# Optimization experiments

Hardware: AMD Instinct MI355X
Metric: run time of the kernel (lower is better)

## Reference

```python
import jax, jax.numpy as jnp
import numpy as np

B, S, D, H = 4, 2048, 1024, 16
HD = D // H  # head dim = 64


def setup_inputs() -> dict:
    key = jax.random.key(0)
    ks = jax.random.split(key, 10)
    sd = 1.0 / np.sqrt(D)
    return {
        "x": jax.random.normal(ks[0], (B, S, D), jnp.float32),
        "Wq": jax.random.normal(ks[1], (D, D), jnp.float32) * sd,
        "Wk": jax.random.normal(ks[2], (D, D), jnp.float32) * sd,
        "Wv": jax.random.normal(ks[3], (D, D), jnp.float32) * sd,
        "in_w": jax.random.normal(ks[4], (3 * D, D), jnp.float32) * sd,
        "in_b": jax.random.normal(ks[5], (3 * D,), jnp.float32) * 0.01,
        "out_w": jax.random.normal(ks[6], (D, D), jnp.float32) * sd,
        "out_b": jax.random.normal(ks[7], (D,), jnp.float32) * 0.01,
        "proj_w": jax.random.normal(ks[8], (D, D), jnp.float32) * sd,
        "proj_b": jax.random.normal(ks[9], (D,), jnp.float32) * 0.01,
    }


def _attn_block(x, Wq, Wk, Wv, in_w, in_b, out_w, out_b, proj_w, proj_b):
    b, s, d = x.shape
    # redundant pre-projections (bias-free)
    q = jnp.einsum('bsd,ed->bse', x, Wq)
    k = jnp.einsum('bsd,ed->bse', x, Wk)
    v = jnp.einsum('bsd,ed->bse', x, Wv)
    # MultiheadAttention internal in-projection (with bias)
    wq, wk, wv = in_w[:d], in_w[d:2 * d], in_w[2 * d:]
    bq, bk, bv = in_b[:d], in_b[d:2 * d], in_b[2 * d:]
    Q = jnp.einsum('bse,fe->bsf', q, wq) + bq
    K = jnp.einsum('bse,fe->bsf', k, wk) + bk
    V = jnp.einsum('bse,fe->bsf', v, wv) + bv
    # split heads -> [b, h, s, hd]
    Q = Q.reshape(b, s, H, HD).transpose(0, 2, 1, 3)
    K = K.reshape(b, s, H, HD).transpose(0, 2, 1, 3)
    V = V.reshape(b, s, H, HD).transpose(0, 2, 1, 3)
    scale = 1.0 / np.sqrt(HD)
    scores = jnp.einsum('bhqd,bhkd->bhqk', Q * scale, K)
    # FAITHFUL quirk: float tril mask (ones / zeros) is ADDED to scores,
    # exactly as torch does with a float attn_mask (not a -inf causal mask).
    mask = jnp.tril(jnp.ones((s, s), scores.dtype))
    scores = scores + mask
    A = jax.nn.softmax(scores, axis=-1)
    ctx = jnp.einsum('bhqk,bhkd->bhqd', A, V)
    ctx = ctx.transpose(0, 2, 1, 3).reshape(b, s, d)
    attn = jnp.einsum('bse,fe->bsf', ctx, out_w) + out_b  # out_proj
    out = jnp.einsum('bse,fe->bsf', attn, proj_w) + proj_b  # self.project
    return x + out


def reference(x, Wq, Wk, Wv, in_w, in_b, out_w, out_b, proj_w, proj_b):
    return _attn_block(x, Wq, Wk, Wv, in_w, in_b, out_w, out_b, proj_w, proj_b)
```

## Files before the change

### kernel.cpp

```cpp
#include <hip/hip_runtime.h>
#include <stdint.h>

typedef unsigned short u16;
typedef __attribute__((ext_vector_type(8))) short bfx8;
typedef __attribute__((ext_vector_type(4))) float fx4;
typedef __attribute__((ext_vector_type(2))) unsigned int uint32x2;

static __device__ __forceinline__ u16 f2b(float f) {
  union { float f; uint32_t u; } v; v.f = f;
  uint32_t r = v.u + 0x7fffu + ((v.u >> 16) & 1u);
  return (u16)(r >> 16);
}

static __device__ __forceinline__ uint32_t cvtpk(float lo, float hi) {
  uint32_t r;
  asm("v_cvt_pk_bf16_f32 %0, %1, %2" : "=v"(r) : "v"(lo), "v"(hi));
  return r;
}

static __device__ __forceinline__ float ex2(float x) {
  float r;
  asm("v_exp_f32 %0, %1" : "=v"(r) : "v"(x));
  return r;
}

static __device__ __forceinline__ void gload16(const void* g, void* lds) {
  __builtin_amdgcn_global_load_lds((const __attribute__((address_space(1))) uint32_t*)g,
                                   (__attribute__((address_space(3))) uint32_t*)lds,
                                   16, 0, 0);
}

__global__ __launch_bounds__(256) void f32_to_bf16_k(const float* __restrict__ in,
                                                     u16* __restrict__ out, int n) {
  int i = (blockIdx.x * 256 + threadIdx.x) * 8;
  if (i >= n) return;
  float4 a = *(const float4*)(in + i);
  float4 b = *(const float4*)(in + i + 4);
  bfx8 o;
  o[0]=(short)f2b(a.x); o[1]=(short)f2b(a.y); o[2]=(short)f2b(a.z); o[3]=(short)f2b(a.w);
  o[4]=(short)f2b(b.x); o[5]=(short)f2b(b.y); o[6]=(short)f2b(b.z); o[7]=(short)f2b(b.w);
  *(bfx8*)(out + i) = o;
}

struct TransArgs { const float* in[4]; u16* out[4]; };
__global__ __launch_bounds__(256) void transpose4_k(TransArgs ta) {
  const float* in = ta.in[blockIdx.z];
  u16* out = ta.out[blockIdx.z];
  __shared__ u16 t[64][65];
  const int bx = blockIdx.x * 64, by = blockIdx.y * 64;
  const int tid = threadIdx.x;
#pragma unroll
  for (int i = 0; i < 16; ++i) {
    int idx = tid + i * 256; int r = idx >> 6, c = idx & 63;
    t[c][r] = f2b(in[(size_t)(by + r) * 1024 + bx + c]);
  }
  __syncthreads();
#pragma unroll
  for (int i = 0; i < 16; ++i) {
    int idx = tid + i * 256; int r = idx >> 6, c = idx & 63;
    out[(size_t)(bx + r) * 1024 + by + c] = t[r][c];
  }
}

__global__ __launch_bounds__(256) void make_b2_k(const float* __restrict__ pw,
                                                 const float* __restrict__ ob,
                                                 const float* __restrict__ pb,
                                                 float* __restrict__ b2) {
  const int f = blockIdx.x, tid = threadIdx.x;
  float s = 0.f;
  for (int e = tid; e < 1024; e += 256) s += pw[(size_t)f * 1024 + e] * ob[e];
#pragma unroll
  for (int d = 1; d < 64; d <<= 1) s += __shfl_xor(s, d);
  __shared__ float red[4];
  if ((tid & 63) == 0) red[tid >> 6] = s;
  __syncthreads();
  if (tid == 0) b2[f] = red[0] + red[1] + red[2] + red[3] + pb[f];
}

static __device__ __forceinline__ void gemm_core(const u16* __restrict__ A,
                                                 const u16* __restrict__ Bt,
                                                 int K, int bm, int bn,
                                                 u16* As, u16* Bs, fx4 (&acc)[4][4]) {
  const int tid = threadIdx.x, w = tid >> 6, l = tid & 63, lm = l & 15, lk = l >> 4;
  const int wm = w >> 1, wn = w & 1;
  const int nkt = K >> 6;
  for (int kt = 0; kt < nkt; ++kt) {
#pragma unroll
    for (int i = 0; i < 4; ++i) {
      int off = i * 4096 + w * 1024;
      int loff = off + l * 16;
      int row = loff >> 7, cb = loff & 127;
      gload16((const char*)A + ((size_t)(bm * 128 + row) * K + kt * 64) * 2 + cb,
              (char*)As + off);
      gload16((const char*)Bt + ((size_t)(bn * 128 + row) * K + kt * 64) * 2 + cb,
              (char*)Bs + off);
    }
    __syncthreads();
#pragma unroll
    for (int kk = 0; kk < 2; ++kk) {
      bfx8 a[4], b[4];
#pragma unroll
      for (int mi = 0; mi < 4; ++mi)
        a[mi] = *(const bfx8*)((const char*)As + (wm * 64 + mi * 16 + lm) * 128 + lk * 16 + kk * 64);
#pragma unroll
      for (int nj = 0; nj < 4; ++nj)
        b[nj] = *(const bfx8*)((const char*)Bs + (wn * 64 + nj * 16 + lm) * 128 + lk * 16 + kk * 64);
#pragma unroll
      for (int mi = 0; mi < 4; ++mi)
#pragma unroll
        for (int nj = 0; nj < 4; ++nj)
          acc[mi][nj] = __builtin_amdgcn_mfma_f32_16x16x32_bf16(a[mi], b[nj], acc[mi][nj], 0, 0, 0);
    }
    __syncthreads();
  }
}

struct CombArgs { const u16* A[4]; const u16* Bt[4]; u16* C[4]; };
__global__ __launch_bounds__(256) void gemm_combine_k(CombArgs ca) {
  const int z = blockIdx.z;
  __shared__ u16 As[8192], Bs[8192];
  fx4 acc[4][4];
#pragma unroll
  for (int mi = 0; mi < 4; ++mi)
#pragma unroll
    for (int nj = 0; nj < 4; ++nj) acc[mi][nj] = 0.f;
  gemm_core(ca.A[z], ca.Bt[z], 1024, blockIdx.x, blockIdx.y, As, Bs, acc);
  const int tid = threadIdx.x, w = tid >> 6, l = tid & 63, lm = l & 15, lk = l >> 4;
  const int wm = w >> 1, wn = w & 1;
  u16* C = ca.C[z];
#pragma unroll
  for (int mi = 0; mi < 4; ++mi)
#pragma unroll
    for (int nj = 0; nj < 4; ++nj)
#pragma unroll
      for (int r = 0; r < 4; ++r) {
        int m = blockIdx.x * 128 + wm * 64 + mi * 16 + lk * 4 + r;
        int n = blockIdx.y * 128 + wn * 64 + nj * 16 + lm;
        C[(size_t)m * 1024 + n] = f2b(acc[mi][nj][r]);
      }
}

__global__ __launch_bounds__(256) void gemm_qkv_k(const u16* __restrict__ xb,
                                                  const u16* __restrict__ Wc,
                                                  const float* __restrict__ bias,
                                                  u16* __restrict__ Qh, u16* __restrict__ Kh,
                                                  u16* __restrict__ Vh) {
  __shared__ u16 As[8192], Bs[8192];
  fx4 acc[4][4];
#pragma unroll
  for (int mi = 0; mi < 4; ++mi)
#pragma unroll
    for (int nj = 0; nj < 4; ++nj) acc[mi][nj] = 0.f;
  gemm_core(xb, Wc, 1024, blockIdx.x, blockIdx.y, As, Bs, acc);
  const int tid = threadIdx.x, w = tid >> 6, l = tid & 63, lm = l & 15, lk = l >> 4;
  const int wm = w >> 1, wn = w & 1;
  const int t = (blockIdx.y * 128) >> 10;
  u16* dst = (t == 0) ? Qh : ((t == 1) ? Kh : Vh);
#pragma unroll
  for (int mi = 0; mi < 4; ++mi)
#pragma unroll
    for (int nj = 0; nj < 4; ++nj)
#pragma unroll
      for (int r = 0; r < 4; ++r) {
        int m = blockIdx.x * 128 + wm * 64 + mi * 16 + lk * 4 + r;
        int n = blockIdx.y * 128 + wn * 64 + nj * 16 + lm;
        float v = acc[mi][nj][r] + bias[n];
        int f = n & 1023, h = f >> 6, hd = f & 63, b = m >> 11, s = m & 2047;
        size_t hb = ((size_t)(b * 16 + h)) * 131072;
        size_t idx;
        if (t == 2) {
          int sl = s & 63, st = s >> 6;
          idx = hb + (size_t)st * 4096 +
                (size_t)((sl >> 2) * 256 + (hd >> 4) * 64 + (sl & 3) * 16 + (hd & 15));
        } else if (t == 1) {
          idx = hb + (size_t)s * 64 + (hd ^ ((s & 7) << 3));
        } else {
          idx = hb + (size_t)s * 64 + hd;
        }
        dst[idx] = f2b(v);
      }
}

__global__ __launch_bounds__(256) void gemm_final_k(const u16* __restrict__ ctx,
                                                    const u16* __restrict__ W2,
                                                    const float* __restrict__ b2,
                                                    const float* __restrict__ x,
                                                    float* __restrict__ out) {
  __shared__ u16 As[8192], Bs[8192];
  fx4 acc[4][4];
#pragma unroll
  for (int mi = 0; mi < 4; ++mi)
#pragma unroll
    for (int nj = 0; nj < 4; ++nj) acc[mi][nj] = 0.f;
  gemm_core(ctx, W2, 1024, blockIdx.x, blockIdx.y, As, Bs, acc);
  const int tid = threadIdx.x, w = tid >> 6, l = tid & 63, lm = l & 15, lk = l >> 4;
  const int wm = w >> 1, wn = w & 1;
#pragma unroll
  for (int mi = 0; mi < 4; ++mi)
#pragma unroll
    for (int nj = 0; nj < 4; ++nj)
#pragma unroll
      for (int r = 0; r < 4; ++r) {
        int m = blockIdx.x * 128 + wm * 64 + mi * 16 + lk * 4 + r;
        int n = blockIdx.y * 128 + wn * 64 + nj * 16 + lm;
        size_t idx = (size_t)m * 1024 + n;
        out[idx] = acc[mi][nj][r] + b2[n] + x[idx];
      }
}

#define TRRD(d, IMM) asm volatile("ds_read_b64_tr_b16 %0, %1 offset:" IMM : "=v"(d) : "v"(va))

__global__ __launch_bounds__(256) void attn_k(const u16* __restrict__ Qh,
                                              const u16* __restrict__ Kh,
                                              const u16* __restrict__ Vh,
                                              u16* __restrict__ ctx) {
  const int bl = blockIdx.x;
  const int wk = (bl & 7) * 128 + (bl >> 3);
  const int bh = wk >> 4, qt = wk & 15;
  const int tid = threadIdx.x, w = tid >> 6, l = tid & 63, lm = l & 15, lk = l >> 4;
  __shared__ __align__(16) u16 Ks[3][4096];
  __shared__ __align__(16) u16 Vs[3][4096];
  __shared__ __align__(16) u16 Pl[4][1024];

  const float SC = 0.18033688011112042f;
  const float MA = 1.4426950408889634f;
  const float THR = 11.541560327111708f;

  const size_t base = (size_t)bh * 131072;
  bfx8 qf[2][2];
#pragma unroll
  for (int g = 0; g < 2; ++g) {
    const u16* qp = Qh + base + (size_t)(qt * 128 + g * 64 + w * 16 + lm) * 64;
    qf[g][0] = *(const bfx8*)(qp + lk * 8);
    qf[g][1] = *(const bfx8*)(qp + lk * 8 + 32);
  }
  float m_run[2] = {-INFINITY, -INFINITY};
  float l_part[2] = {0.f, 0.f};
  fx4 accO[2][4];
#pragma unroll
  for (int g = 0; g < 2; ++g)
#pragma unroll
    for (int nj = 0; nj < 4; ++nj) accO[g][nj] = 0.f;

  const char* Kg = (const char*)(Kh + base);
  const char* Vg = (const char*)(Vh + base);
  const int o0 = w * 1024 + l * 16, o1 = o0 + 4096;

  const int swz = (lm & 7) << 4;
  const uint32_t vs_base =
      (uint32_t)(uintptr_t)(__attribute__((address_space(3))) char*)&Vs[0][0];
  const uint32_t vtrb = vs_base + (uint32_t)(lk * 1024 + lm * 8);

#define STAGE(t, s)                                        \
  {                                                        \
    const char* kg_ = Kg + (t) * 8192;                     \
    const char* vg_ = Vg + (t) * 8192;                     \
    gload16(kg_ + o0, (char*)Ks[s] + o0);                  \
    gload16(kg_ + o1, (char*)Ks[s] + o1);                  \
    gload16(vg_ + o0, (char*)Vs[s] + o0);                  \
    gload16(vg_ + o1, (char*)Vs[s] + o1);                  \
  }

  STAGE(0, 0);
  STAGE(1, 1);
  asm volatile("s_waitcnt vmcnt(4)" ::: "memory");
  __builtin_amdgcn_s_barrier();
  __builtin_amdgcn_sched_barrier(0);

  int s0 = 0, s1 = 1, s2 = 2;
  for (int kt = 0; kt < 32; ++kt) {
    if (kt + 2 < 32) STAGE(kt + 2, s2);
    __builtin_amdgcn_sched_barrier(0);

    const char* Kc = (const char*)Ks[s0];
    fx4 s[2][4];
#pragma unroll
    for (int g = 0; g < 2; ++g)
#pragma unroll
      for (int nj = 0; nj < 4; ++nj) s[g][nj] = 0.f;
    __builtin_amdgcn_s_setprio(1);
#pragma unroll
    for (int kk = 0; kk < 2; ++kk) {
      bfx8 kf[4];
#pragma unroll
      for (int nj = 0; nj < 4; ++nj)
        kf[nj] = *(const bfx8*)(Kc + nj * 2048 + lm * 128 +
                                (((kk * 4 + lk) ^ (lm & 7)) << 4));
#pragma unroll
      for (int g = 0; g < 2; ++g)
#pragma unroll
        for (int nj = 0; nj < 4; ++nj)
          s[g][nj] = __builtin_amdgcn_mfma_f32_16x16x32_bf16(kf[nj], qf[g][kk], s[g][nj], 0, 0, 0);
    }
    __builtin_amdgcn_s_setprio(0);
#pragma unroll
    for (int g = 0; g < 2; ++g) {
      const int dk = kt - 2 * qt - g;
      if (dk < 0) {
#pragma unroll
        for (int nj = 0; nj < 4; ++nj)
#pragma unroll
          for (int r = 0; r < 4; ++r) s[g][nj][r] = fmaf(s[g][nj][r], SC, MA);
      } else if (dk > 0) {
#pragma unroll
        for (int nj = 0; nj < 4; ++nj)
#pragma unroll
          for (int r = 0; r < 4; ++r) s[g][nj][r] *= SC;
      } else {
        const int qg = qt * 128 + g * 64 + w * 16 + lm;
#pragma unroll
        for (int nj = 0; nj < 4; ++nj)
#pragma unroll
          for (int r = 0; r < 4; ++r) {
            int key = kt * 64 + nj * 16 + lk * 4 + r;
            s[g][nj][r] = s[g][nj][r] * SC + ((key <= qg) ? MA : 0.0f);
          }
      }
      float mx = fmaxf(fmaxf(fmaxf(s[g][0][0], s[g][0][1]), fmaxf(s[g][0][2], s[g][0][3])),
                       fmaxf(fmaxf(s[g][1][0], s[g][1][1]), fmaxf(s[g][1][2], s[g][1][3])));
      mx = fmaxf(mx, fmaxf(fmaxf(fmaxf(s[g][2][0], s[g][2][1]), fmaxf(s[g][2][2], s[g][2][3])),
                           fmaxf(fmaxf(s[g][3][0], s[g][3][1]), fmaxf(s[g][3][2], s[g][3][3]))));
      if (!__all(mx <= m_run[g] + THR)) {
        mx = fmaxf(mx, __shfl_xor(mx, 16));
        mx = fmaxf(mx, __shfl_xor(mx, 32));
        float mn = fmaxf(m_run[g], mx);
        float corr = ex2(m_run[g] - mn);
        m_run[g] = mn;
        l_part[g] *= corr;
#pragma unroll
        for (int r = 0; r < 4; ++r) {
          float cr = __shfl(corr, (l & 48) | (lk * 4 + r));
#pragma unroll
          for (int nj = 0; nj < 4; ++nj) accO[g][nj][r] *= cr;
        }
      }
      float lsum = 0.f;
#pragma unroll
      for (int nj = 0; nj < 4; ++nj)
#pragma unroll
        for (int r = 0; r < 4; ++r) {
          float p = ex2(s[g][nj][r] - m_run[g]);
          s[g][nj][r] = p;
          lsum += p;
        }
      l_part[g] += lsum;
    }
#pragma unroll
    for (int nj = 0; nj < 4; ++nj) {
      uint32x2 pw;
      pw[0] = cvtpk(s[0][nj][0], s[0][nj][1]);
      pw[1] = cvtpk(s[0][nj][2], s[0][nj][3]);
      *(uint32x2*)((char*)Pl[w] + ((lm * 128 + nj * 32 + lk * 8) ^ swz)) = pw;
    }
    uint32x2 tr[2][4][2];
    uint32_t va = vtrb + (uint32_t)(s0 * 8192);
    TRRD(tr[0][0][0], "0");    TRRD(tr[0][0][1], "512");
    TRRD(tr[0][1][0], "128");  TRRD(tr[0][1][1], "640");
    TRRD(tr[0][2][0], "256");  TRRD(tr[0][2][1], "768");
    TRRD(tr[0][3][0], "384");  TRRD(tr[0][3][1], "896");
    TRRD(tr[1][0][0], "4096"); TRRD(tr[1][0][1], "4608");
    TRRD(tr[1][1][0], "4224"); TRRD(tr[1][1][1], "4736");
    TRRD(tr[1][2][0], "4352"); TRRD(tr[1][2][1], "4864");
    TRRD(tr[1][3][0], "4480"); TRRD(tr[1][3][1], "4992");
    asm volatile("s_waitcnt lgkmcnt(0)" ::: "memory");
    __builtin_amdgcn_sched_barrier(0);
    __builtin_amdgcn_s_setprio(1);
#pragma unroll
    for (int kk = 0; kk < 2; ++kk) {
      bfx8 pf = *(const bfx8*)((char*)Pl[w] + ((lm * 128 + kk * 64 + lk * 16) ^ swz));
#pragma unroll
      for (int nj = 0; nj < 4; ++nj) {
        union { uint32x2 u2[2]; bfx8 v; } u;
        u.u2[0] = tr[kk][nj][0];
        u.u2[1] = tr[kk][nj][1];
        accO[0][nj] = __builtin_amdgcn_mfma_f32_16x16x32_bf16(pf, u.v, accO[0][nj], 0, 0, 0);
      }
    }
    __builtin_amdgcn_s_setprio(0);
#pragma unroll
    for (int nj = 0; nj < 4; ++nj) {
      uint32x2 pw;
      pw[0] = cvtpk(s[1][nj][0], s[1][nj][1]);
      pw[1] = cvtpk(s[1][nj][2], s[1][nj][3]);
      *(uint32x2*)((char*)Pl[w] + ((lm * 128 + nj * 32 + lk * 8) ^ swz)) = pw;
    }
    __builtin_amdgcn_s_setprio(1);
#pragma unroll
    for (int kk = 0; kk < 2; ++kk) {
      bfx8 pf = *(const bfx8*)((char*)Pl[w] + ((lm * 128 + kk * 64 + lk * 16) ^ swz));
#pragma unroll
      for (int nj = 0; nj < 4; ++nj) {
        union { uint32x2 u2[2]; bfx8 v; } u;
        u.u2[0] = tr[kk][nj][0];
        u.u2[1] = tr[kk][nj][1];
        accO[1][nj] = __builtin_amdgcn_mfma_f32_16x16x32_bf16(pf, u.v, accO[1][nj], 0, 0, 0);
      }
    }
    __builtin_amdgcn_s_setprio(0);

    if (kt < 31) {
      if (kt < 30) asm volatile("s_waitcnt vmcnt(4)" ::: "memory");
      else         asm volatile("s_waitcnt vmcnt(0)" ::: "memory");
      __builtin_amdgcn_s_barrier();
      __builtin_amdgcn_sched_barrier(0);
    }
    int tswp = s0; s0 = s1; s1 = s2; s2 = tswp;
  }
#undef STAGE

  const int b = bh >> 4, h = bh & 15;
#pragma unroll
  for (int g = 0; g < 2; ++g) {
    float lt = l_part[g];
    lt += __shfl_xor(lt, 16);
    lt += __shfl_xor(lt, 32);
#pragma unroll
    for (int r = 0; r < 4; ++r) {
      float li = __shfl(lt, (l & 48) | (lk * 4 + r));
      float inv = 1.0f / li;
      int q = qt * 128 + g * 64 + w * 16 + lk * 4 + r;
#pragma unroll
      for (int nj = 0; nj < 4; ++nj)
        ctx[((size_t)b * 2048 + q) * 1024 + h * 64 + nj * 16 + lm] = f2b(accO[g][nj][r] * inv);
    }
  }
}

extern "C" void kernel_launch(void* const* d_in, const int* in_sizes, int n_in,
                              void* d_out, int out_size, void* d_ws, size_t ws_size,
                              hipStream_t stream) {
  (void)in_sizes; (void)n_in; (void)out_size; (void)ws_size;
  const float* x      = (const float*)d_in[0];
  const float* Wq     = (const float*)d_in[1];
  const float* Wk     = (const float*)d_in[2];
  const float* Wv     = (const float*)d_in[3];
  const float* in_w   = (const float*)d_in[4];
  const float* in_b   = (const float*)d_in[5];
  const float* out_w  = (const float*)d_in[6];
  const float* out_b  = (const float*)d_in[7];
  const float* proj_w = (const float*)d_in[8];
  const float* proj_b = (const float*)d_in[9];
  float* out = (float*)d_out;

  char* ws = (char*)d_ws;
  const size_t MB = 1ull << 20;
  u16* xb   = (u16*)(ws);
  u16* ctx  = xb;
  u16* Qh   = (u16*)(ws + 16 * MB);
  u16* Kh   = (u16*)(ws + 32 * MB);
  u16* Vh   = (u16*)(ws + 48 * MB);
  u16* inwb = Kh;
  u16* tmpT = Vh;
  u16* pwb  = (u16*)(ws + 48 * MB + 8 * MB);
  u16* Wc   = (u16*)(ws + 64 * MB);
  u16* W2   = (u16*)(ws + 70 * MB);
  float* b2 = (float*)(ws + 72 * MB);

  f32_to_bf16_k<<<4096, 256, 0, stream>>>(x, xb, 8388608);
  f32_to_bf16_k<<<1536, 256, 0, stream>>>(in_w, inwb, 3145728);
  f32_to_bf16_k<<<512, 256, 0, stream>>>(proj_w, pwb, 1048576);

  TransArgs ta;
  ta.in[0] = Wq; ta.in[1] = Wk; ta.in[2] = Wv; ta.in[3] = out_w;
  for (int z = 0; z < 4; ++z) ta.out[z] = tmpT + (size_t)z * 1048576;
  transpose4_k<<<dim3(16, 16, 4), 256, 0, stream>>>(ta);

  CombArgs ca;
  ca.A[0] = inwb; ca.A[1] = inwb + 1048576; ca.A[2] = inwb + 2097152; ca.A[3] = pwb;
  for (int z = 0; z < 4; ++z) ca.Bt[z] = tmpT + (size_t)z * 1048576;
  ca.C[0] = Wc; ca.C[1] = Wc + 1048576; ca.C[2] = Wc + 2097152; ca.C[3] = W2;
  gemm_combine_k<<<dim3(8, 8, 4), 256, 0, stream>>>(ca);

  make_b2_k<<<1024, 256, 0, stream>>>(proj_w, out_b, proj_b, b2);

  gemm_qkv_k<<<dim3(64, 24), 256, 0, stream>>>(xb, Wc, in_b, Qh, Kh, Vh);
  attn_k<<<1024, 256, 0, stream>>>(Qh, Kh, Vh, ctx);
  gemm_final_k<<<dim3(64, 8), 256, 0, stream>>>(ctx, W2, b2, x, out);
}
```

Measured before the change: 294.3 us.

## Enlarge attention blocks to 8 waves, pre-transpose V, fold max into FMA

The attention kernel now uses 512-thread blocks covering 256 queries, so each K/V tile staged in LDS serves twice as many query rows. V is written by the QKV GEMM in a transposed, XOR-swizzled layout, which lets the kernel read V fragments with plain vector LDS loads instead of ds_read_b64_tr_b16. The running-max subtraction is folded into the scale FMA, with a finite initial max and a delta-based rescale. The trade-offs are fewer blocks in the grid, higher register pressure under launch_bounds(512,4), and a coupled layout change between the two kernels.

```diff
diff --git a/kernel.cpp b/kernel.cpp
--- a/kernel.cpp
+++ b/kernel.cpp
@@ -170,8 +170,7 @@
         size_t idx;
         if (t == 2) {
           int sl = s & 63, st = s >> 6;
-          idx = hb + (size_t)st * 4096 +
-                (size_t)((sl >> 2) * 256 + (hd >> 4) * 64 + (sl & 3) * 16 + (hd & 15));
+          idx = hb + (size_t)st * 4096 + (size_t)(hd * 64 + (sl ^ ((hd & 7) << 3)));
         } else if (t == 1) {
           idx = hb + (size_t)s * 64 + (hd ^ ((s & 7) << 3));
         } else {
@@ -208,33 +207,32 @@
       }
 }
 
-#define TRRD(d, IMM) asm volatile("ds_read_b64_tr_b16 %0, %1 offset:" IMM : "=v"(d) : "v"(va))
-
-__global__ __launch_bounds__(256) void attn_k(const u16* __restrict__ Qh,
-                                              const u16* __restrict__ Kh,
-                                              const u16* __restrict__ Vh,
-                                              u16* __restrict__ ctx) {
+__global__ __launch_bounds__(512, 4) void attn_k(const u16* __restrict__ Qh,
+                                                 const u16* __restrict__ Kh,
+                                                 const u16* __restrict__ Vh,
+                                                 u16* __restrict__ ctx) {
   const int bl = blockIdx.x;
-  const int wk = (bl & 7) * 128 + (bl >> 3);
-  const int bh = wk >> 4, qt = wk & 15;
+  const int wk = (bl & 7) * 64 + (bl >> 3);
+  const int bh = wk >> 3, qt = wk & 7;
   const int tid = threadIdx.x, w = tid >> 6, l = tid & 63, lm = l & 15, lk = l >> 4;
   __shared__ __align__(16) u16 Ks[3][4096];
   __shared__ __align__(16) u16 Vs[3][4096];
-  __shared__ __align__(16) u16 Pl[4][1024];
+  __shared__ __align__(16) u16 Pl[8][1024];
 
   const float SC = 0.18033688011112042f;
   const float MA = 1.4426950408889634f;
   const float THR = 11.541560327111708f;
 
   const size_t base = (size_t)bh * 131072;
+  const int gb0 = qt * 256 + w * 32;
   bfx8 qf[2][2];
 #pragma unroll
   for (int g = 0; g < 2; ++g) {
-    const u16* qp = Qh + base + (size_t)(qt * 128 + g * 64 + w * 16 + lm) * 64;
+    const u16* qp = Qh + base + (size_t)(gb0 + g * 16 + lm) * 64;
     qf[g][0] = *(const bfx8*)(qp + lk * 8);
     qf[g][1] = *(const bfx8*)(qp + lk * 8 + 32);
   }
-  float m_run[2] = {-INFINITY, -INFINITY};
+  float m_run[2] = {-1024.f, -1024.f};
   float l_part[2] = {0.f, 0.f};
   fx4 accO[2][4];
 #pragma unroll
@@ -244,26 +242,18 @@
 
   const char* Kg = (const char*)(Kh + base);
   const char* Vg = (const char*)(Vh + base);
-  const int o0 = w * 1024 + l * 16, o1 = o0 + 4096;
-
+  const int o = tid * 16;
   const int swz = (lm & 7) << 4;
-  const uint32_t vs_base =
-      (uint32_t)(uintptr_t)(__attribute__((address_space(3))) char*)&Vs[0][0];
-  const uint32_t vtrb = vs_base + (uint32_t)(lk * 1024 + lm * 8);
-
-#define STAGE(t, s)                                        \
-  {                                                        \
-    const char* kg_ = Kg + (t) * 8192;                     \
-    const char* vg_ = Vg + (t) * 8192;                     \
-    gload16(kg_ + o0, (char*)Ks[s] + o0);                  \
-    gload16(kg_ + o1, (char*)Ks[s] + o1);                  \
-    gload16(vg_ + o0, (char*)Vs[s] + o0);                  \
-    gload16(vg_ + o1, (char*)Vs[s] + o1);                  \
+
+#define STAGE(t, s)                                          \
+  {                                                          \
+    gload16(Kg + (size_t)(t) * 8192 + o, (char*)Ks[s] + o);  \
+    gload16(Vg + (size_t)(t) * 8192 + o, (char*)Vs[s] + o);  \
   }
 
   STAGE(0, 0);
   STAGE(1, 1);
-  asm volatile("s_waitcnt vmcnt(4)" ::: "memory");
+  asm volatile("s_waitcnt vmcnt(2)" ::: "memory");
   __builtin_amdgcn_s_barrier();
   __builtin_amdgcn_sched_barrier(0);
 
@@ -273,11 +263,12 @@
     __builtin_amdgcn_sched_barrier(0);
 
     const char* Kc = (const char*)Ks[s0];
-    fx4 s[2][4];
+    const char* Vc = (const char*)Vs[s0];
+    fx4 sg[2][4];
 #pragma unroll
     for (int g = 0; g < 2; ++g)
 #pragma unroll
-      for (int nj = 0; nj < 4; ++nj) s[g][nj] = 0.f;
+      for (int nj = 0; nj < 4; ++nj) sg[g][nj] = 0.f;
     __builtin_amdgcn_s_setprio(1);
 #pragma unroll
     for (int kk = 0; kk < 2; ++kk) {
@@ -290,42 +281,44 @@
       for (int g = 0; g < 2; ++g)
 #pragma unroll
         for (int nj = 0; nj < 4; ++nj)
-          s[g][nj] = __builtin_amdgcn_mfma_f32_16x16x32_bf16(kf[nj], qf[g][kk], s[g][nj], 0, 0, 0);
+          sg[g][nj] = __builtin_amdgcn_mfma_f32_16x16x32_bf16(kf[nj], qf[g][kk], sg[g][nj], 0, 0, 0);
     }
     __builtin_amdgcn_s_setprio(0);
+
 #pragma unroll
     for (int g = 0; g < 2; ++g) {
-      const int dk = kt - 2 * qt - g;
+      const int dk = kt - ((gb0 + g * 16) >> 6);
+      float cO = -m_run[g], cI = cO + MA;
       if (dk < 0) {
 #pragma unroll
         for (int nj = 0; nj < 4; ++nj)
 #pragma unroll
-          for (int r = 0; r < 4; ++r) s[g][nj][r] = fmaf(s[g][nj][r], SC, MA);
+          for (int r = 0; r < 4; ++r) sg[g][nj][r] = fmaf(sg[g][nj][r], SC, cI);
       } else if (dk > 0) {
 #pragma unroll
         for (int nj = 0; nj < 4; ++nj)
 #pragma unroll
-          for (int r = 0; r < 4; ++r) s[g][nj][r] *= SC;
+          for (int r = 0; r < 4; ++r) sg[g][nj][r] = fmaf(sg[g][nj][r], SC, cO);
       } else {
-        const int qg = qt * 128 + g * 64 + w * 16 + lm;
+        const int qg = gb0 + g * 16 + lm;
 #pragma unroll
         for (int nj = 0; nj < 4; ++nj)
 #pragma unroll
           for (int r = 0; r < 4; ++r) {
             int key = kt * 64 + nj * 16 + lk * 4 + r;
-            s[g][nj][r] = s[g][nj][r] * SC + ((key <= qg) ? MA : 0.0f);
+            sg[g][nj][r] = fmaf(sg[g][nj][r], SC, (key <= qg) ? cI : cO);
           }
       }
-      float mx = fmaxf(fmaxf(fmaxf(s[g][0][0], s[g][0][1]), fmaxf(s[g][0][2], s[g][0][3])),
-                       fmaxf(fmaxf(s[g][1][0], s[g][1][1]), fmaxf(s[g][1][2], s[g][1][3])));
-      mx = fmaxf(mx, fmaxf(fmaxf(fmaxf(s[g][2][0], s[g][2][1]), fmaxf(s[g][2][2], s[g][2][3])),
-                           fmaxf(fmaxf(s[g][3][0], s[g][3][1]), fmaxf(s[g][3][2], s[g][3][3]))));
-      if (!__all(mx <= m_run[g] + THR)) {
-        mx = fmaxf(mx, __shfl_xor(mx, 16));
-        mx = fmaxf(mx, __shfl_xor(mx, 32));
-        float mn = fmaxf(m_run[g], mx);
-        float corr = ex2(m_run[g] - mn);
-        m_run[g] = mn;
+      float mx = fmaxf(fmaxf(fmaxf(sg[g][0][0], sg[g][0][1]), fmaxf(sg[g][0][2], sg[g][0][3])),
+                       fmaxf(fmaxf(sg[g][1][0], sg[g][1][1]), fmaxf(sg[g][1][2], sg[g][1][3])));
+      mx = fmaxf(mx, fmaxf(fmaxf(fmaxf(sg[g][2][0], sg[g][2][1]), fmaxf(sg[g][2][2], sg[g][2][3])),
+                           fmaxf(fmaxf(sg[g][3][0], sg[g][3][1]), fmaxf(sg[g][3][2], sg[g][3][3]))));
+      if (!__all(mx <= THR)) {
+        float mxr = fmaxf(mx, __shfl_xor(mx, 16));
+        mxr = fmaxf(mxr, __shfl_xor(mxr, 32));
+        float d = fmaxf(mxr, 0.f);
+        float corr = ex2(-d);
+        m_run[g] += d;
         l_part[g] *= corr;
 #pragma unroll
         for (int r = 0; r < 4; ++r) {
@@ -333,55 +326,51 @@
 #pragma unroll
           for (int nj = 0; nj < 4; ++nj) accO[g][nj][r] *= cr;
         }
+#pragma unroll
+        for (int nj = 0; nj < 4; ++nj)
+#pragma unroll
+          for (int r = 0; r < 4; ++r) sg[g][nj][r] -= d;
       }
       float lsum = 0.f;
 #pragma unroll
       for (int nj = 0; nj < 4; ++nj)
 #pragma unroll
         for (int r = 0; r < 4; ++r) {
-          float p = ex2(s[g][nj][r] - m_run[g]);
-          s[g][nj][r] = p;
+          float p = ex2(sg[g][nj][r]);
+          sg[g][nj][r] = p;
           lsum += p;
         }
       l_part[g] += lsum;
     }
+
 #pragma unroll
     for (int nj = 0; nj < 4; ++nj) {
       uint32x2 pw;
-      pw[0] = cvtpk(s[0][nj][0], s[0][nj][1]);
-      pw[1] = cvtpk(s[0][nj][2], s[0][nj][3]);
+      pw[0] = cvtpk(sg[0][nj][0], sg[0][nj][1]);
+      pw[1] = cvtpk(sg[0][nj][2], sg[0][nj][3]);
       *(uint32x2*)((char*)Pl[w] + ((lm * 128 + nj * 32 + lk * 8) ^ swz)) = pw;
     }
-    uint32x2 tr[2][4][2];
-    uint32_t va = vtrb + (uint32_t)(s0 * 8192);
-    TRRD(tr[0][0][0], "0");    TRRD(tr[0][0][1], "512");
-    TRRD(tr[0][1][0], "128");  TRRD(tr[0][1][1], "640");
-    TRRD(tr[0][2][0], "256");  TRRD(tr[0][2][1], "768");
-    TRRD(tr[0][3][0], "384");  TRRD(tr[0][3][1], "896");
-    TRRD(tr[1][0][0], "4096"); TRRD(tr[1][0][1], "4608");
-    TRRD(tr[1][1][0], "4224"); TRRD(tr[1][1][1], "4736");
-    TRRD(tr[1][2][0], "4352"); TRRD(tr[1][2][1], "4864");
-    TRRD(tr[1][3][0], "4480"); TRRD(tr[1][3][1], "4992");
-    asm volatile("s_waitcnt lgkmcnt(0)" ::: "memory");
-    __builtin_amdgcn_sched_barrier(0);
+    bfx8 vf[2][4];
+#pragma unroll
+    for (int kk = 0; kk < 2; ++kk)
+#pragma unroll
+      for (int nj = 0; nj < 4; ++nj)
+        vf[kk][nj] = *(const bfx8*)(Vc + nj * 2048 + lm * 128 +
+                                    (((kk * 4 + lk) ^ (lm & 7)) << 4));
     __builtin_amdgcn_s_setprio(1);
 #pragma unroll
     for (int kk = 0; kk < 2; ++kk) {
       bfx8 pf = *(const bfx8*)((char*)Pl[w] + ((lm * 128 + kk * 64 + lk * 16) ^ swz));
 #pragma unroll
-      for (int nj = 0; nj < 4; ++nj) {
-        union { uint32x2 u2[2]; bfx8 v; } u;
-        u.u2[0] = tr[kk][nj][0];
-        u.u2[1] = tr[kk][nj][1];
-        accO[0][nj] = __builtin_amdgcn_mfma_f32_16x16x32_bf16(pf, u.v, accO[0][nj], 0, 0, 0);
-      }
+      for (int nj = 0; nj < 4; ++nj)
+        accO[0][nj] = __builtin_amdgcn_mfma_f32_16x16x32_bf16(pf, vf[kk][nj], accO[0][nj], 0, 0, 0);
     }
     __builtin_amdgcn_s_setprio(0);
 #pragma unroll
     for (int nj = 0; nj < 4; ++nj) {
       uint32x2 pw;
-      pw[0] = cvtpk(s[1][nj][0], s[1][nj][1]);
-      pw[1] = cvtpk(s[1][nj][2], s[1][nj][3]);
+      pw[0] = cvtpk(sg[1][nj][0], sg[1][nj][1]);
+      pw[1] = cvtpk(sg[1][nj][2], sg[1][nj][3]);
       *(uint32x2*)((char*)Pl[w] + ((lm * 128 + nj * 32 + lk * 8) ^ swz)) = pw;
     }
     __builtin_amdgcn_s_setprio(1);
@@ -389,17 +378,13 @@
     for (int kk = 0; kk < 2; ++kk) {
       bfx8 pf = *(const bfx8*)((char*)Pl[w] + ((lm * 128 + kk * 64 + lk * 16) ^ swz));
 #pragma unroll
-      for (int nj = 0; nj < 4; ++nj) {
-        union { uint32x2 u2[2]; bfx8 v; } u;
-        u.u2[0] = tr[kk][nj][0];
-        u.u2[1] = tr[kk][nj][1];
-        accO[1][nj] = __builtin_amdgcn_mfma_f32_16x16x32_bf16(pf, u.v, accO[1][nj], 0, 0, 0);
-      }
+      for (int nj = 0; nj < 4; ++nj)
+        accO[1][nj] = __builtin_amdgcn_mfma_f32_16x16x32_bf16(pf, vf[kk][nj], accO[1][nj], 0, 0, 0);
     }
     __builtin_amdgcn_s_setprio(0);
 
     if (kt < 31) {
-      if (kt < 30) asm volatile("s_waitcnt vmcnt(4)" ::: "memory");
+      if (kt < 30) asm volatile("s_waitcnt vmcnt(2)" ::: "memory");
       else         asm volatile("s_waitcnt vmcnt(0)" ::: "memory");
       __builtin_amdgcn_s_barrier();
       __builtin_amdgcn_sched_barrier(0);
@@ -418,7 +403,7 @@
     for (int r = 0; r < 4; ++r) {
       float li = __shfl(lt, (l & 48) | (lk * 4 + r));
       float inv = 1.0f / li;
-      int q = qt * 128 + g * 64 + w * 16 + lk * 4 + r;
+      int q = gb0 + g * 16 + lk * 4 + r;
 #pragma unroll
       for (int nj = 0; nj < 4; ++nj)
         ctx[((size_t)b * 2048 + q) * 1024 + h * 64 + nj * 16 + lm] = f2b(accO[g][nj][r] * inv);
@@ -474,6 +459,6 @@
   make_b2_k<<<1024, 256, 0, stream>>>(proj_w, out_b, proj_b, b2);
 
   gemm_qkv_k<<<dim3(64, 24), 256, 0, stream>>>(xb, Wc, in_b, Qh, Kh, Vh);
-  attn_k<<<1024, 256, 0, stream>>>(Qh, Kh, Vh, ctx);
+  attn_k<<<512, 512, 0, stream>>>(Qh, Kh, Vh, ctx);
   gemm_final_k<<<dim3(64, 8), 256, 0, stream>>>(ctx, W2, b2, x, out);
 }
```

Result: faster. 286.3 us (-2.7%).
